# Kernel optimization log

Measured on AMD Instinct MI355X. Metric: run time of the kernel, lower is better.

The kernel has to match this reference:

```python
import jax, jax.numpy as jnp
import numpy as np
from jax import lax

B, C, H, W = 4, 256, 64, 64
R = 4  # reduction
BN_EPS = 1e-5


def setup_inputs() -> dict:
    key = jax.random.key(0)
    ks = jax.random.split(key, 18)
    n = jax.random.normal
    return {
        "x_self": n(ks[0], (B, C, H, W), jnp.float32),
        "x_other": n(ks[1], (B, C, H, W), jnp.float32),
        "q_w": n(ks[2], (C, C), jnp.float32) * 0.05,      # self_q 1x1 conv
        "q_b": n(ks[3], (C,), jnp.float32) * 0.05,
        "kv_w": n(ks[4], (2 * C, C), jnp.float32) * 0.05,  # other_kv 1x1 conv
        "kv_b": n(ks[5], (2 * C,), jnp.float32) * 0.05,
        "g1_w": n(ks[6], (C // R, C), jnp.float32) * 0.05,  # gate conv1
        "g1_b": n(ks[7], (C // R,), jnp.float32) * 0.05,
        "g2_w": n(ks[8], (1, C // R), jnp.float32) * 0.05,  # gate conv2
        "g2_b": n(ks[9], (1,), jnp.float32) * 0.05,
        "dw_w": n(ks[10], (C, 1, 3, 3), jnp.float32) * 0.1,  # depthwise 3x3
        "dw_b": n(ks[11], (C,), jnp.float32) * 0.05,
        "bn_g": jnp.ones((C,), jnp.float32),
        "bn_b": jnp.zeros((C,), jnp.float32),
        "bn_m": n(ks[12], (C,), jnp.float32) * 0.05,
        "bn_v": jax.random.uniform(ks[13], (C,), jnp.float32, 0.5, 1.5),
        "out_w": n(ks[14], (C, C), jnp.float32) * 0.05,
        "out_b": n(ks[15], (C,), jnp.float32) * 0.05,
    }


def _conv1x1(x, w, b):
    return jnp.einsum('bchw,oc->bohw', x, w) + b[None, :, None, None]


def reference(x_self, x_other, q_w, q_b, kv_w, kv_b, g1_w, g1_b, g2_w, g2_b,
              dw_w, dw_b, bn_g, bn_b, bn_m, bn_v, out_w, out_b):
    # local branch: depthwise 3x3 conv -> BatchNorm (eval stats) -> SiLU
    y = lax.conv_general_dilated(
        x_self, dw_w, (1, 1), 'SAME',
        feature_group_count=C,
        dimension_numbers=('NCHW', 'OIHW', 'NCHW')) + dw_b[None, :, None, None]
    scale = (bn_g / jnp.sqrt(bn_v + BN_EPS))[None, :, None, None]
    y = (y - bn_m[None, :, None, None]) * scale + bn_b[None, :, None, None]
    local_feat = y * jax.nn.sigmoid(y)  # SiLU

    # cross attention over HW tokens
    q = _conv1x1(x_self, q_w, q_b).reshape(B, C, H * W)
    kv = _conv1x1(x_other, kv_w, kv_b)
    k = kv[:, :C].reshape(B, C, H * W)
    v = kv[:, C:].reshape(B, C, H * W)
    attn = jnp.einsum('bcn,bcm->bnm', q, k) / jnp.sqrt(jnp.float32(C))  # [B,HW,HW]
    attn = jax.nn.softmax(attn, axis=-1)
    attn_out = jnp.einsum('bnm,bcm->bcn', attn, v).reshape(B, C, H, W)

    # channel-squeeze gate on x_self -> scalar per sample
    p = jnp.mean(x_self, axis=(2, 3))                 # [B,C] global avg pool
    g = jax.nn.relu(p @ g1_w.T + g1_b)                # [B,C//R]
    g = jax.nn.sigmoid(g @ g2_w.T + g2_b)             # [B,1]
    gate = g[:, :, None, None]

    fused = local_feat + gate * attn_out
    return _conv1x1(fused, out_w, out_b)
```

## Files before the change

### kernel.cpp

```cpp
#include <hip/hip_runtime.h>
#include <stdint.h>

#define BB 4
#define CC 256
#define HH 64
#define WWD 64
#define NN 4096
#define LOG2E 1.4426950408889634f

typedef __attribute__((ext_vector_type(8))) short short8;
typedef __attribute__((ext_vector_type(4))) float f32x4;
typedef __attribute__((ext_vector_type(16))) float f32x16;
typedef __attribute__((ext_vector_type(4))) unsigned short us4;
typedef unsigned long long ull;

__device__ __forceinline__ unsigned short f2bf(float f) {
  unsigned int u = __float_as_uint(f);
  u += 0x7fffu + ((u >> 16) & 1u);
  return (unsigned short)(u >> 16);
}
__device__ __forceinline__ float bf2f(unsigned short h) {
  return __uint_as_float(((unsigned int)h) << 16);
}
__device__ __forceinline__ short8 ld8(const unsigned short* p) {
  return *reinterpret_cast<const short8*>(p);
}
__device__ __forceinline__ unsigned char f2fp8(float v) {
  return (unsigned char)__builtin_amdgcn_cvt_pk_fp8_f32(v, v, 0, false);
}
__device__ __forceinline__ int rowmap(int reg, int h) {
  return (reg & 3) + 8 * (reg >> 2) + 4 * h;
}

__global__ __launch_bounds__(256, 2) void k_pre(
    const float* __restrict__ xs, const float* __restrict__ xo,
    const float* __restrict__ dww, const float* __restrict__ dwb,
    const float* __restrict__ bng, const float* __restrict__ bnb,
    const float* __restrict__ bnm, const float* __restrict__ bnv,
    const float* __restrict__ qw, const float* __restrict__ kvw,
    const float* __restrict__ ow, unsigned short* __restrict__ XtS,
    unsigned short* __restrict__ XtO, unsigned short* __restrict__ localT,
    float* __restrict__ psumA, unsigned short* __restrict__ Wb) {
  __shared__ float rb3[3][64][67];
  __shared__ unsigned short sb[64][67];
  int tid = threadIdx.x;
  if (blockIdx.z == 8) {
    int i = (blockIdx.x * 64 + blockIdx.y) * 1024 + tid * 4;
    const float* src;
    if (i < 65536) src = qw + i;
    else if (i < 196608) src = kvw + (i - 65536);
    else src = ow + (i - 196608);
    f32x4 v = *reinterpret_cast<const f32x4*>(src);
    us4 r;
#pragma unroll
    for (int j = 0; j < 4; ++j) r[j] = f2bf(v[j]);
    *reinterpret_cast<us4*>(Wb + i) = r;
    return;
  }
  int c0 = blockIdx.x * 64, h = blockIdx.y;
  int b = blockIdx.z >> 1, which = blockIdx.z & 1;
  const float* src = which ? xo : xs;
  int wq = tid >> 6, w = tid & 63;
  int dlo = which ? 1 : 0, dhi = which ? 1 : 2;
  for (int d = dlo; d <= dhi; ++d) {
    int hh = h + d - 1;
    bool ok = (hh >= 0 && hh < HH);
#pragma unroll
    for (int p = 0; p < 4; ++p) {
      int idx = p * 256 + tid;
      int cl = idx >> 4, ws4 = (idx & 15) * 4;
      f32x4 v = {};
      if (ok)
        v = *reinterpret_cast<const f32x4*>(
            &src[(((size_t)(b * CC + c0 + cl)) * HH + hh) * WWD + ws4]);
#pragma unroll
      for (int j = 0; j < 4; ++j) rb3[d][cl][ws4 + 1 + j] = v[j];
    }
    if (tid < 64) { rb3[d][tid][0] = 0.f; rb3[d][tid][65] = 0.f; }
  }
  __syncthreads();
  unsigned short* dst = which ? XtO : XtS;
  int n0 = h * 64, cb = (tid & 15) * 4;
#pragma unroll
  for (int i = 0; i < 4; ++i) {
    int wl = i * 16 + (tid >> 4);
    us4 r;
#pragma unroll
    for (int j = 0; j < 4; ++j) r[j] = f2bf(rb3[1][cb + j][wl + 1]);
    *reinterpret_cast<us4*>(&dst[((size_t)b * NN + n0 + wl) * CC + c0 + cb]) = r;
  }
  if (which) return;
  if (tid < 64) {
    float s = 0.f;
    for (int ww = 0; ww < 64; ++ww) s += rb3[1][tid][ww + 1];
    psumA[((size_t)(b * 64 + h)) * CC + c0 + tid] = s;
  }
  for (int p = 0; p < 16; ++p) {
    int cl = p * 4 + wq, c = c0 + cl;
    float acc = 0.f;
#pragma unroll
    for (int di = 0; di < 3; ++di)
#pragma unroll
      for (int dj = 0; dj < 3; ++dj)
        acc = fmaf(rb3[di][cl][w + dj], dww[c * 9 + di * 3 + dj], acc);
    float y = acc + dwb[c];
    float sc = bng[c] * rsqrtf(bnv[c] + 1e-5f);
    float v = (y - bnm[c]) * sc + bnb[c];
    sb[cl][w] = f2bf(v / (1.f + __expf(-v)));
  }
  __syncthreads();
#pragma unroll
  for (int i = 0; i < 4; ++i) {
    int wl = i * 16 + (tid >> 4);
    us4 r;
#pragma unroll
    for (int j = 0; j < 4; ++j) r[j] = sb[cb + j][wl];
    *reinterpret_cast<us4*>(&localT[((size_t)b * NN + h * WWD + wl) * CC + c0 + cb]) = r;
  }
}

__global__ __launch_bounds__(256, 4) void k_qkv(
    const unsigned short* __restrict__ XtS, const unsigned short* __restrict__ XtO,
    const unsigned short* __restrict__ Wb, const float* __restrict__ qb,
    const float* __restrict__ kvb, const float* __restrict__ psumA,
    const float* __restrict__ g1w, const float* __restrict__ g1b,
    const float* __restrict__ g2w, const float* __restrict__ g2b,
    unsigned char* __restrict__ Qt8, unsigned char* __restrict__ Kt8,
    unsigned char* __restrict__ Vv8, float* __restrict__ gate) {
  __shared__ unsigned short Xs[64][264];
  int tid = threadIdx.x;
  int id = blockIdx.y;
  if (id == 3) {
    if (blockIdx.x != 0 || blockIdx.z != 0) return;
    float* mf = (float*)&Xs[0][0];
    float* hpf = mf + 1024;
    int c = tid;
    for (int b4 = 0; b4 < 4; ++b4) {
      float s = 0.f;
      for (int hh = 0; hh < 64; ++hh) s += psumA[((size_t)(b4 * 64 + hh)) * CC + c];
      mf[b4 * 256 + c] = s * (1.f / 4096.f);
    }
    __syncthreads();
    for (int b4 = 0; b4 < 4; ++b4) {
      int j = tid >> 2, cq = tid & 3;
      float s = 0.f;
      for (int cc = cq * 64; cc < cq * 64 + 64; ++cc)
        s = fmaf(mf[b4 * 256 + cc], g1w[j * CC + cc], s);
      hpf[j * 5 + cq] = s;
      __syncthreads();
      if (tid < 64) {
        float hh = fmaxf(hpf[tid * 5] + hpf[tid * 5 + 1] + hpf[tid * 5 + 2] +
                             hpf[tid * 5 + 3] + g1b[tid], 0.f);
        float t = hh * g2w[tid];
        for (int off = 32; off; off >>= 1) t += __shfl_down(t, off, 64);
        if (tid == 0) gate[b4] = 1.f / (1.f + expf(-(t + g2b[0])));
      }
      __syncthreads();
    }
    return;
  }
  int n0 = blockIdx.x * 64, b = blockIdx.z;
  const unsigned short* Xt = (id == 0) ? XtS : XtO;
  const unsigned short* W = Wb + id * 65536;
  int wave = tid >> 6, lane = tid & 63, l31 = lane & 31, h = lane >> 5;
#pragma unroll
  for (int p = 0; p < 8; ++p) {
    int r = p * 8 + (tid >> 5), c = (tid & 31) * 8;
    *reinterpret_cast<uint4*>(&Xs[r][c]) =
        *reinterpret_cast<const uint4*>(Xt + ((size_t)b * NN + n0 + r) * CC + c);
  }
  __syncthreads();
  int o0 = wave * 64;
  f32x16 acc[4] = {};
  if (id < 2) {
#pragma unroll
    for (int t = 0; t < 16; ++t) {
      short8 a0 = ld8(&Xs[l31][t * 16 + h * 8]);
      short8 a1 = ld8(&Xs[32 + l31][t * 16 + h * 8]);
      short8 b0 = ld8(W + (size_t)(o0 + l31) * CC + t * 16 + h * 8);
      short8 b1 = ld8(W + (size_t)(o0 + 32 + l31) * CC + t * 16 + h * 8);
      acc[0] = __builtin_amdgcn_mfma_f32_32x32x16_bf16(a0, b0, acc[0], 0, 0, 0);
      acc[1] = __builtin_amdgcn_mfma_f32_32x32x16_bf16(a0, b1, acc[1], 0, 0, 0);
      acc[2] = __builtin_amdgcn_mfma_f32_32x32x16_bf16(a1, b0, acc[2], 0, 0, 0);
      acc[3] = __builtin_amdgcn_mfma_f32_32x32x16_bf16(a1, b1, acc[3], 0, 0, 0);
    }
    const float* bias = id ? kvb : qb;
    __syncthreads();
    unsigned char (*T8)[264] = reinterpret_cast<unsigned char(*)[264]>(&Xs[0][0]);
#pragma unroll
    for (int nt = 0; nt < 2; ++nt)
#pragma unroll
      for (int ot = 0; ot < 2; ++ot) {
        int o = o0 + ot * 32 + l31;
        float bv = bias[o];
#pragma unroll
        for (int reg = 0; reg < 16; ++reg) {
          int nl = nt * 32 + rowmap(reg, h);
          T8[nl][o] = f2fp8((acc[nt * 2 + ot][reg] + bv) * 0.25f);
        }
      }
    __syncthreads();
    if (id == 0) {
#pragma unroll
      for (int p = 0; p < 4; ++p) {
        int idx = p * 256 + tid, row = idx >> 4, cc = (idx & 15) * 16;
        ull a0 = *reinterpret_cast<const ull*>(&T8[row][cc]);
        ull a1 = *reinterpret_cast<const ull*>(&T8[row][cc + 8]);
        uint4 u;
        u.x = (unsigned)a0; u.y = (unsigned)(a0 >> 32);
        u.z = (unsigned)a1; u.w = (unsigned)(a1 >> 32);
        *reinterpret_cast<uint4*>(Qt8 + ((size_t)b * NN + n0 + row) * CC + cc) = u;
      }
    } else {
      size_t tb = ((size_t)b * 32 + (n0 >> 7)) * 32768 + (size_t)(n0 & 64) * 8;
#pragma unroll
      for (int p = 0; p < 8; ++p) {
        int ch = p * 256 + tid;
        int m = ch & 63, s2 = ch >> 6;
        *reinterpret_cast<ull*>(Kt8 + tb + (size_t)s2 * 1024 + m * 8) =
            *reinterpret_cast<const ull*>(&T8[m][s2 * 8]);
      }
    }
  } else {
#pragma unroll
    for (int t = 0; t < 16; ++t) {
      short8 a0 = ld8(W + (size_t)(o0 + l31) * CC + t * 16 + h * 8);
      short8 a1 = ld8(W + (size_t)(o0 + 32 + l31) * CC + t * 16 + h * 8);
      short8 b0 = ld8(&Xs[l31][t * 16 + h * 8]);
      short8 b1 = ld8(&Xs[32 + l31][t * 16 + h * 8]);
      acc[0] = __builtin_amdgcn_mfma_f32_32x32x16_bf16(a0, b0, acc[0], 0, 0, 0);
      acc[1] = __builtin_amdgcn_mfma_f32_32x32x16_bf16(a0, b1, acc[1], 0, 0, 0);
      acc[2] = __builtin_amdgcn_mfma_f32_32x32x16_bf16(a1, b0, acc[2], 0, 0, 0);
      acc[3] = __builtin_amdgcn_mfma_f32_32x32x16_bf16(a1, b1, acc[3], 0, 0, 0);
    }
    __syncthreads();
    unsigned char (*V8)[72] = reinterpret_cast<unsigned char(*)[72]>(&Xs[0][0]);
#pragma unroll
    for (int ot = 0; ot < 2; ++ot)
#pragma unroll
      for (int nt = 0; nt < 2; ++nt)
#pragma unroll
        for (int reg = 0; reg < 16; ++reg) {
          int o = o0 + ot * 32 + rowmap(reg, h);
          int nl = nt * 32 + l31;
          V8[o][nl] = f2fp8(acc[ot * 2 + nt][reg] + kvb[CC + o]);
        }
    __syncthreads();
    size_t tb = ((size_t)b * 32 + (n0 >> 7)) * 32768 + (size_t)((n0 & 64) >> 3) * 2048;
#pragma unroll
    for (int p = 0; p < 8; ++p) {
      int ch = p * 256 + tid;
      int c = ch & 255, svl = ch >> 8;
      *reinterpret_cast<ull*>(Vv8 + tb + (size_t)svl * 2048 + c * 8) =
          *reinterpret_cast<const ull*>(&V8[c][svl * 8]);
    }
  }
}

__global__ __launch_bounds__(256, 3) void k_flash8(
    const unsigned char* __restrict__ Qt8, const unsigned char* __restrict__ Kd,
    const unsigned char* __restrict__ Vd, const unsigned short* __restrict__ localT,
    const float* __restrict__ gate, unsigned short* __restrict__ OpartA,
    unsigned short* __restrict__ OpartB,
    float* __restrict__ Lpart, unsigned short* __restrict__ fusedT) {
  __shared__ unsigned char Ps8[64][136];
  __shared__ float lred[2][64];
  int b = blockIdx.x & 3, n0 = (blockIdx.x >> 2) * 64;
  int sp = blockIdx.y, nsp = gridDim.y;
  int tid = threadIdx.x, wave = tid >> 6, lane = tid & 63, l31 = lane & 31, h = lane >> 5;
  int rw = wave & 1, cw = wave >> 1;
  const unsigned char* qp = Qt8 + ((size_t)b * NN + n0 + rw * 32 + l31) * CC + h * 8;
  long qf[16];
#pragma unroll
  for (int t = 0; t < 16; ++t) qf[t] = *reinterpret_cast<const long*>(qp + t * 16);
  f32x16 O[4] = {};
  float lsum = 0.f;
  int m_lo = (32 * sp) / nsp, m_hi = (32 * (sp + 1)) / nsp;
  const unsigned char* Kb = Kd + (size_t)b * (32u * 32768u);
  const unsigned char* Vb = Vd + (size_t)b * (32u * 32768u);
  for (int mt = m_lo; mt < m_hi; ++mt) {
    const unsigned char* Kq = Kb + (size_t)mt * 32768 + h * 1024 + (cw * 64 + l31) * 8;
    f32x16 Sa = {}, Sb = {};
    __builtin_amdgcn_s_setprio(1);
#pragma unroll
    for (int t = 0; t < 16; ++t) {
      long kfa = *reinterpret_cast<const long*>(Kq + (size_t)t * 2048);
      long kfb = *reinterpret_cast<const long*>(Kq + (size_t)t * 2048 + 256);
      Sa = __builtin_amdgcn_mfma_f32_32x32x16_fp8_fp8(kfa, qf[t], Sa, 0, 0, 0);
      Sb = __builtin_amdgcn_mfma_f32_32x32x16_fp8_fp8(kfb, qf[t], Sb, 0, 0, 0);
    }
    __builtin_amdgcn_s_setprio(0);
#pragma unroll
    for (int r = 0; r < 4; ++r) {
      float p0 = __builtin_exp2f(Sa[4 * r + 0] * LOG2E);
      float p1 = __builtin_exp2f(Sa[4 * r + 1] * LOG2E);
      float p2 = __builtin_exp2f(Sa[4 * r + 2] * LOG2E);
      float p3 = __builtin_exp2f(Sa[4 * r + 3] * LOG2E);
      lsum += (p0 + p1) + (p2 + p3);
      unsigned u = __builtin_amdgcn_cvt_pk_fp8_f32(p0, p1, 0, false);
      u = __builtin_amdgcn_cvt_pk_fp8_f32(p2, p3, u, true);
      *reinterpret_cast<unsigned*>(&Ps8[rw * 32 + l31][cw * 64 + 8 * r + 4 * h]) = u;
      float q0 = __builtin_exp2f(Sb[4 * r + 0] * LOG2E);
      float q1 = __builtin_exp2f(Sb[4 * r + 1] * LOG2E);
      float q2 = __builtin_exp2f(Sb[4 * r + 2] * LOG2E);
      float q3 = __builtin_exp2f(Sb[4 * r + 3] * LOG2E);
      lsum += (q0 + q1) + (q2 + q3);
      unsigned u2 = __builtin_amdgcn_cvt_pk_fp8_f32(q0, q1, 0, false);
      u2 = __builtin_amdgcn_cvt_pk_fp8_f32(q2, q3, u2, true);
      *reinterpret_cast<unsigned*>(&Ps8[rw * 32 + l31][cw * 64 + 32 + 8 * r + 4 * h]) = u2;
    }
    asm volatile("s_waitcnt lgkmcnt(0)" ::: "memory");
    __builtin_amdgcn_s_barrier();
    __builtin_amdgcn_sched_barrier(0);
    const unsigned char* Vq = Vb + (size_t)mt * 32768 + h * 2048 + (cw * 128 + l31) * 8;
    __builtin_amdgcn_s_setprio(1);
#pragma unroll
    for (int t = 0; t < 8; ++t) {
      long pf = *reinterpret_cast<const long*>(&Ps8[rw * 32 + l31][t * 16 + h * 8]);
#pragma unroll
      for (int ct = 0; ct < 4; ++ct) {
        long vf = *reinterpret_cast<const long*>(Vq + (size_t)t * 4096 + ct * 256);
        O[ct] = __builtin_amdgcn_mfma_f32_32x32x16_fp8_fp8(pf, vf, O[ct], 0, 0, 0);
      }
    }
    __builtin_amdgcn_s_setprio(0);
    __builtin_amdgcn_s_barrier();
  }
  lsum += __shfl_xor(lsum, 32, 64);
  __syncthreads();
  if (h == 0) lred[cw][rw * 32 + l31] = lsum;
  __syncthreads();
  if (nsp == 1) {
    float* ltot = reinterpret_cast<float*>(&Ps8[0][0]);
    if (tid < 64) ltot[tid] = lred[0][tid] + lred[1][tid];
    __syncthreads();
    float gv = gate[b];
    float inv[16];
#pragma unroll
    for (int reg = 0; reg < 16; ++reg)
      inv[reg] = gv / ltot[rw * 32 + rowmap(reg, h)];
#pragma unroll
    for (int ct = 0; ct < 4; ++ct)
#pragma unroll
      for (int reg = 0; reg < 16; ++reg) {
        int n = n0 + rw * 32 + rowmap(reg, h);
        int c = cw * 128 + ct * 32 + l31;
        size_t idx = ((size_t)b * NN + n) * CC + c;
        fusedT[idx] = f2bf(bf2f(localT[idx]) + O[ct][reg] * inv[reg]);
      }
  } else {
    if (tid < 64) Lpart[(size_t)(b * nsp + sp) * NN + n0 + tid] = lred[0][tid] + lred[1][tid];
    unsigned short* Op;
    size_t slab;
    if (sp == 0) { Op = OpartA; slab = (size_t)b * NN; }
    else { Op = OpartB; slab = (size_t)(b * (nsp - 1) + (sp - 1)) * NN; }
#pragma unroll
    for (int ct = 0; ct < 4; ++ct)
#pragma unroll
      for (int reg = 0; reg < 16; ++reg) {
        int n = n0 + rw * 32 + rowmap(reg, h);
        int c = cw * 128 + ct * 32 + l31;
        Op[(slab + n) * CC + c] = f2bf(O[ct][reg]);
      }
  }
}

__global__ __launch_bounds__(256, 4) void k_out(
    const unsigned short* __restrict__ W, const float* __restrict__ ob,
    const float* __restrict__ gate, const unsigned short* __restrict__ localT,
    const unsigned short* __restrict__ OpartA, const unsigned short* __restrict__ OpartB,
    const float* __restrict__ Lpart,
    const unsigned short* __restrict__ fusedT, float* __restrict__ out, int nsp) {
  __shared__ unsigned short Xs[64][264];
  int n0 = blockIdx.x * 64, o0 = blockIdx.y * 128, b = blockIdx.z;
  int tid = threadIdx.x, wave = tid >> 6, lane = tid & 63, l31 = lane & 31, h = lane >> 5;
  if (nsp > 1) {
    float gv = gate[b];
#pragma unroll
    for (int p = 0; p < 8; ++p) {
      int r = p * 8 + (tid >> 5), cc = (tid & 31) * 8;
      int n = n0 + r;
      float lsum = 0.f;
      for (int sp = 0; sp < nsp; ++sp) lsum += Lpart[(size_t)(b * nsp + sp) * NN + n];
      float g = gv / lsum;
      float ov[8] = {};
      for (int sp = 0; sp < nsp; ++sp) {
        const unsigned short* Op;
        size_t slab;
        if (sp == 0) { Op = OpartA; slab = (size_t)b * NN; }
        else { Op = OpartB; slab = (size_t)(b * (nsp - 1) + (sp - 1)) * NN; }
        short8 x = ld8(Op + (slab + n) * CC + cc);
#pragma unroll
        for (int j = 0; j < 8; ++j) ov[j] += bf2f(((unsigned short*)&x)[j]);
      }
      const unsigned short* lp = localT + ((size_t)b * NN + n) * CC + cc;
      short8 lv = ld8(lp);
      us4 r0, r1;
#pragma unroll
      for (int j = 0; j < 4; ++j) {
        r0[j] = f2bf(bf2f(((unsigned short*)&lv)[j]) + ov[j] * g);
        r1[j] = f2bf(bf2f(((unsigned short*)&lv)[j + 4]) + ov[j + 4] * g);
      }
      *reinterpret_cast<us4*>(&Xs[r][cc]) = r0;
      *reinterpret_cast<us4*>(&Xs[r][cc + 4]) = r1;
    }
  } else {
#pragma unroll
    for (int p = 0; p < 8; ++p) {
      int r = p * 8 + (tid >> 5), c = (tid & 31) * 8;
      *reinterpret_cast<uint4*>(&Xs[r][c]) =
          *reinterpret_cast<const uint4*>(fusedT + ((size_t)b * NN + n0 + r) * CC + c);
    }
  }
  int obase = o0 + wave * 32;
  short8 af[16];
#pragma unroll
  for (int t = 0; t < 16; ++t) af[t] = ld8(W + (size_t)(obase + l31) * CC + t * 16 + h * 8);
  __syncthreads();
  f32x16 acc[2] = {};
#pragma unroll
  for (int t = 0; t < 16; ++t) {
    short8 b0 = ld8(&Xs[l31][t * 16 + h * 8]);
    short8 b1 = ld8(&Xs[32 + l31][t * 16 + h * 8]);
    acc[0] = __builtin_amdgcn_mfma_f32_32x32x16_bf16(af[t], b0, acc[0], 0, 0, 0);
    acc[1] = __builtin_amdgcn_mfma_f32_32x32x16_bf16(af[t], b1, acc[1], 0, 0, 0);
  }
#pragma unroll
  for (int nt = 0; nt < 2; ++nt)
#pragma unroll
    for (int reg = 0; reg < 16; ++reg) {
      int o = obase + rowmap(reg, h);
      int n = n0 + nt * 32 + l31;
      out[((size_t)b * CC + o) * NN + n] = acc[nt][reg] + ob[o];
    }
}

extern "C" void kernel_launch(void* const* d_in, const int* in_sizes, int n_in,
                              void* d_out, int out_size, void* d_ws, size_t ws_size,
                              hipStream_t stream) {
  const float* xs  = (const float*)d_in[0];
  const float* xo  = (const float*)d_in[1];
  const float* qw  = (const float*)d_in[2];
  const float* qb  = (const float*)d_in[3];
  const float* kvw = (const float*)d_in[4];
  const float* kvb = (const float*)d_in[5];
  const float* g1w = (const float*)d_in[6];
  const float* g1b = (const float*)d_in[7];
  const float* g2w = (const float*)d_in[8];
  const float* g2b = (const float*)d_in[9];
  const float* dww = (const float*)d_in[10];
  const float* dwb = (const float*)d_in[11];
  const float* bng = (const float*)d_in[12];
  const float* bnb = (const float*)d_in[13];
  const float* bnm = (const float*)d_in[14];
  const float* bnv = (const float*)d_in[15];
  const float* ow  = (const float*)d_in[16];
  const float* ob  = (const float*)d_in[17];
  float* out = (float*)d_out;
  char* ws = (char*)d_ws;

  const size_t SZ  = (size_t)BB * NN * CC * 2;
  const size_t SZ8 = (size_t)BB * NN * CC;
  unsigned short* XtS    = (unsigned short*)(ws);
  unsigned short* XtO    = (unsigned short*)(ws + SZ);
  unsigned short* localT = (unsigned short*)(ws + 2 * SZ);
  unsigned char*  Qt8    = (unsigned char*)(ws + 3 * SZ);
  unsigned char*  Kt8    = (unsigned char*)(ws + 3 * SZ + SZ8);
  unsigned char*  Vv8    = (unsigned char*)(ws + 3 * SZ + 2 * SZ8);
  unsigned short* Wb     = (unsigned short*)(ws + 3 * SZ + 3 * SZ8);
  float* psumA = (float*)(ws + 3 * SZ + 3 * SZ8 + 524288);
  float* gate  = (float*)(ws + 3 * SZ + 3 * SZ8 + 524288 + 262144);
  size_t tail  = 3 * SZ + 3 * SZ8 + 524288 + 262144 + 4096;
  float* Lpart = (float*)(ws + tail);
  unsigned short* OpartA = XtO;
  unsigned short* OpartB = (unsigned short*)(ws + tail + 262144);
  unsigned short* fusedT = XtS;

  size_t base = tail + 262144;
  int S = 1;
  if (ws_size >= base + 2ull * SZ) S = 3;
  else if (ws_size >= base + 1ull * SZ) S = 2;

  k_pre<<<dim3(4, 64, 9), 256, 0, stream>>>(xs, xo, dww, dwb, bng, bnb, bnm, bnv,
                                            qw, kvw, ow, XtS, XtO, localT, psumA, Wb);
  k_qkv<<<dim3(64, 4, 4), 256, 0, stream>>>(XtS, XtO, Wb, qb, kvb, psumA,
                                            g1w, g1b, g2w, g2b, Qt8, Kt8, Vv8, gate);
  k_flash8<<<dim3(256, S), 256, 0, stream>>>(Qt8, Kt8, Vv8, localT, gate, OpartA,
                                             OpartB, Lpart, fusedT);
  k_out<<<dim3(64, 2, 4), 256, 0, stream>>>(Wb + 196608, ob, gate, localT,
                                            OpartA, OpartB, Lpart, fusedT, out, S);
}
```

Before: 250.9 us.

## Feed P directly from registers to PV MFMA and double-buffer the exchange tile

The V tile layout written by the KV projection kernel is permuted so that the S-accumulator register layout of each wave can be used directly as the A operand of the PV MFMA. Each wave multiplies its own P half straight from registers and reads only the other wave's half from double-buffered shared memory. This removes one barrier per tile and half of the LDS round trip for P. In exchange it depends on a subtle permutation of the key index staying consistent between the producer and consumer kernels, and it raises shared memory use.

```diff
diff --git a/kernel.cpp b/kernel.cpp
--- a/kernel.cpp
+++ b/kernel.cpp
@@ -246,13 +246,16 @@
           V8[o][nl] = f2fp8(acc[ot * 2 + nt][reg] + kvb[CC + o]);
         }
     __syncthreads();
-    size_t tb = ((size_t)b * 32 + (n0 >> 7)) * 32768 + (size_t)((n0 & 64) >> 3) * 2048;
+    size_t tb = ((size_t)b * 32 + (n0 >> 7)) * 32768 + (size_t)(n0 & 64) * 256;
 #pragma unroll
     for (int p = 0; p < 8; ++p) {
       int ch = p * 256 + tid;
-      int c = ch & 255, svl = ch >> 8;
-      *reinterpret_cast<ull*>(Vv8 + tb + (size_t)svl * 2048 + c * 8) =
-          *reinterpret_cast<const ull*>(&V8[c][svl * 8]);
+      int c = ch & 255, slot = ch >> 8;
+      int tl = slot >> 1, h2 = slot & 1;
+      unsigned lo = *reinterpret_cast<const unsigned*>(&V8[c][tl * 16 + h2 * 4]);
+      unsigned hi = *reinterpret_cast<const unsigned*>(&V8[c][tl * 16 + 8 + h2 * 4]);
+      ull chunk = (ull)lo | ((ull)hi << 32);
+      *reinterpret_cast<ull*>(Vv8 + tb + (size_t)slot * 2048 + c * 8) = chunk;
     }
   }
 }
@@ -263,7 +266,7 @@
     const float* __restrict__ gate, unsigned short* __restrict__ OpartA,
     unsigned short* __restrict__ OpartB,
     float* __restrict__ Lpart, unsigned short* __restrict__ fusedT) {
-  __shared__ unsigned char Ps8[64][136];
+  __shared__ unsigned char PsD[2][2][2][64][32];
   __shared__ float lred[2][64];
   int b = blockIdx.x & 3, n0 = (blockIdx.x >> 2) * 64;
   int sp = blockIdx.y, nsp = gridDim.y;
@@ -278,6 +281,7 @@
   int m_lo = (32 * sp) / nsp, m_hi = (32 * (sp + 1)) / nsp;
   const unsigned char* Kb = Kd + (size_t)b * (32u * 32768u);
   const unsigned char* Vb = Vd + (size_t)b * (32u * 32768u);
+  int buf = 0;
   for (int mt = m_lo; mt < m_hi; ++mt) {
     const unsigned char* Kq = Kb + (size_t)mt * 32768 + h * 1024 + (cw * 64 + l31) * 8;
     f32x16 Sa = {}, Sb = {};
@@ -290,48 +294,99 @@
       Sb = __builtin_amdgcn_mfma_f32_32x32x16_fp8_fp8(kfb, qf[t], Sb, 0, 0, 0);
     }
     __builtin_amdgcn_s_setprio(0);
-#pragma unroll
-    for (int r = 0; r < 4; ++r) {
-      float p0 = __builtin_exp2f(Sa[4 * r + 0] * LOG2E);
-      float p1 = __builtin_exp2f(Sa[4 * r + 1] * LOG2E);
-      float p2 = __builtin_exp2f(Sa[4 * r + 2] * LOG2E);
-      float p3 = __builtin_exp2f(Sa[4 * r + 3] * LOG2E);
-      lsum += (p0 + p1) + (p2 + p3);
-      unsigned u = __builtin_amdgcn_cvt_pk_fp8_f32(p0, p1, 0, false);
-      u = __builtin_amdgcn_cvt_pk_fp8_f32(p2, p3, u, true);
-      *reinterpret_cast<unsigned*>(&Ps8[rw * 32 + l31][cw * 64 + 8 * r + 4 * h]) = u;
-      float q0 = __builtin_exp2f(Sb[4 * r + 0] * LOG2E);
-      float q1 = __builtin_exp2f(Sb[4 * r + 1] * LOG2E);
-      float q2 = __builtin_exp2f(Sb[4 * r + 2] * LOG2E);
-      float q3 = __builtin_exp2f(Sb[4 * r + 3] * LOG2E);
-      lsum += (q0 + q1) + (q2 + q3);
-      unsigned u2 = __builtin_amdgcn_cvt_pk_fp8_f32(q0, q1, 0, false);
-      u2 = __builtin_amdgcn_cvt_pk_fp8_f32(q2, q3, u2, true);
-      *reinterpret_cast<unsigned*>(&Ps8[rw * 32 + l31][cw * 64 + 32 + 8 * r + 4 * h]) = u2;
-    }
+    unsigned d0, d1, d2, d3, d4, d5, d6, d7;
+    {
+      float e0 = __builtin_exp2f(Sa[0] * LOG2E), e1 = __builtin_exp2f(Sa[1] * LOG2E);
+      float e2 = __builtin_exp2f(Sa[2] * LOG2E), e3 = __builtin_exp2f(Sa[3] * LOG2E);
+      lsum += (e0 + e1) + (e2 + e3);
+      d0 = __builtin_amdgcn_cvt_pk_fp8_f32(e2, e3,
+           __builtin_amdgcn_cvt_pk_fp8_f32(e0, e1, 0, false), true);
+      e0 = __builtin_exp2f(Sa[4] * LOG2E); e1 = __builtin_exp2f(Sa[5] * LOG2E);
+      e2 = __builtin_exp2f(Sa[6] * LOG2E); e3 = __builtin_exp2f(Sa[7] * LOG2E);
+      lsum += (e0 + e1) + (e2 + e3);
+      d1 = __builtin_amdgcn_cvt_pk_fp8_f32(e2, e3,
+           __builtin_amdgcn_cvt_pk_fp8_f32(e0, e1, 0, false), true);
+      e0 = __builtin_exp2f(Sa[8] * LOG2E); e1 = __builtin_exp2f(Sa[9] * LOG2E);
+      e2 = __builtin_exp2f(Sa[10] * LOG2E); e3 = __builtin_exp2f(Sa[11] * LOG2E);
+      lsum += (e0 + e1) + (e2 + e3);
+      d2 = __builtin_amdgcn_cvt_pk_fp8_f32(e2, e3,
+           __builtin_amdgcn_cvt_pk_fp8_f32(e0, e1, 0, false), true);
+      e0 = __builtin_exp2f(Sa[12] * LOG2E); e1 = __builtin_exp2f(Sa[13] * LOG2E);
+      e2 = __builtin_exp2f(Sa[14] * LOG2E); e3 = __builtin_exp2f(Sa[15] * LOG2E);
+      lsum += (e0 + e1) + (e2 + e3);
+      d3 = __builtin_amdgcn_cvt_pk_fp8_f32(e2, e3,
+           __builtin_amdgcn_cvt_pk_fp8_f32(e0, e1, 0, false), true);
+      e0 = __builtin_exp2f(Sb[0] * LOG2E); e1 = __builtin_exp2f(Sb[1] * LOG2E);
+      e2 = __builtin_exp2f(Sb[2] * LOG2E); e3 = __builtin_exp2f(Sb[3] * LOG2E);
+      lsum += (e0 + e1) + (e2 + e3);
+      d4 = __builtin_amdgcn_cvt_pk_fp8_f32(e2, e3,
+           __builtin_amdgcn_cvt_pk_fp8_f32(e0, e1, 0, false), true);
+      e0 = __builtin_exp2f(Sb[4] * LOG2E); e1 = __builtin_exp2f(Sb[5] * LOG2E);
+      e2 = __builtin_exp2f(Sb[6] * LOG2E); e3 = __builtin_exp2f(Sb[7] * LOG2E);
+      lsum += (e0 + e1) + (e2 + e3);
+      d5 = __builtin_amdgcn_cvt_pk_fp8_f32(e2, e3,
+           __builtin_amdgcn_cvt_pk_fp8_f32(e0, e1, 0, false), true);
+      e0 = __builtin_exp2f(Sb[8] * LOG2E); e1 = __builtin_exp2f(Sb[9] * LOG2E);
+      e2 = __builtin_exp2f(Sb[10] * LOG2E); e3 = __builtin_exp2f(Sb[11] * LOG2E);
+      lsum += (e0 + e1) + (e2 + e3);
+      d6 = __builtin_amdgcn_cvt_pk_fp8_f32(e2, e3,
+           __builtin_amdgcn_cvt_pk_fp8_f32(e0, e1, 0, false), true);
+      e0 = __builtin_exp2f(Sb[12] * LOG2E); e1 = __builtin_exp2f(Sb[13] * LOG2E);
+      e2 = __builtin_exp2f(Sb[14] * LOG2E); e3 = __builtin_exp2f(Sb[15] * LOG2E);
+      lsum += (e0 + e1) + (e2 + e3);
+      d7 = __builtin_amdgcn_cvt_pk_fp8_f32(e2, e3,
+           __builtin_amdgcn_cvt_pk_fp8_f32(e0, e1, 0, false), true);
+    }
+    uint4 w0; w0.x = d0; w0.y = d1; w0.z = d2; w0.w = d3;
+    uint4 w1; w1.x = d4; w1.y = d5; w1.z = d6; w1.w = d7;
+    *reinterpret_cast<uint4*>(&PsD[buf][cw][rw][lane][0]) = w0;
+    *reinterpret_cast<uint4*>(&PsD[buf][cw][rw][lane][16]) = w1;
+    const unsigned char* Vq = Vb + (size_t)mt * 32768 + h * 2048 + (cw * 128 + l31) * 8;
+    long pf0 = (long)(((ull)d1 << 32) | d0);
+    long pf1 = (long)(((ull)d3 << 32) | d2);
+    long pf2 = (long)(((ull)d5 << 32) | d4);
+    long pf3 = (long)(((ull)d7 << 32) | d6);
+    __builtin_amdgcn_s_setprio(1);
+#pragma unroll
+    for (int ct = 0; ct < 4; ++ct) {
+      const unsigned char* Vc = Vq + (size_t)(cw * 4) * 4096 + ct * 256;
+      O[ct] = __builtin_amdgcn_mfma_f32_32x32x16_fp8_fp8(
+          pf0, *reinterpret_cast<const long*>(Vc), O[ct], 0, 0, 0);
+      O[ct] = __builtin_amdgcn_mfma_f32_32x32x16_fp8_fp8(
+          pf1, *reinterpret_cast<const long*>(Vc + 4096), O[ct], 0, 0, 0);
+      O[ct] = __builtin_amdgcn_mfma_f32_32x32x16_fp8_fp8(
+          pf2, *reinterpret_cast<const long*>(Vc + 8192), O[ct], 0, 0, 0);
+      O[ct] = __builtin_amdgcn_mfma_f32_32x32x16_fp8_fp8(
+          pf3, *reinterpret_cast<const long*>(Vc + 12288), O[ct], 0, 0, 0);
+    }
+    __builtin_amdgcn_s_setprio(0);
     asm volatile("s_waitcnt lgkmcnt(0)" ::: "memory");
     __builtin_amdgcn_s_barrier();
     __builtin_amdgcn_sched_barrier(0);
-    const unsigned char* Vq = Vb + (size_t)mt * 32768 + h * 2048 + (cw * 128 + l31) * 8;
+    const ull* pp = reinterpret_cast<const ull*>(&PsD[buf][cw ^ 1][rw][lane][0]);
+    ull q0 = pp[0], q1 = pp[1], q2 = pp[2], q3 = pp[3];
     __builtin_amdgcn_s_setprio(1);
 #pragma unroll
-    for (int t = 0; t < 8; ++t) {
-      long pf = *reinterpret_cast<const long*>(&Ps8[rw * 32 + l31][t * 16 + h * 8]);
-#pragma unroll
-      for (int ct = 0; ct < 4; ++ct) {
-        long vf = *reinterpret_cast<const long*>(Vq + (size_t)t * 4096 + ct * 256);
-        O[ct] = __builtin_amdgcn_mfma_f32_32x32x16_fp8_fp8(pf, vf, O[ct], 0, 0, 0);
-      }
+    for (int ct = 0; ct < 4; ++ct) {
+      const unsigned char* Vc = Vq + (size_t)((cw ^ 1) * 4) * 4096 + ct * 256;
+      O[ct] = __builtin_amdgcn_mfma_f32_32x32x16_fp8_fp8(
+          (long)q0, *reinterpret_cast<const long*>(Vc), O[ct], 0, 0, 0);
+      O[ct] = __builtin_amdgcn_mfma_f32_32x32x16_fp8_fp8(
+          (long)q1, *reinterpret_cast<const long*>(Vc + 4096), O[ct], 0, 0, 0);
+      O[ct] = __builtin_amdgcn_mfma_f32_32x32x16_fp8_fp8(
+          (long)q2, *reinterpret_cast<const long*>(Vc + 8192), O[ct], 0, 0, 0);
+      O[ct] = __builtin_amdgcn_mfma_f32_32x32x16_fp8_fp8(
+          (long)q3, *reinterpret_cast<const long*>(Vc + 12288), O[ct], 0, 0, 0);
     }
     __builtin_amdgcn_s_setprio(0);
-    __builtin_amdgcn_s_barrier();
+    buf ^= 1;
   }
   lsum += __shfl_xor(lsum, 32, 64);
   __syncthreads();
   if (h == 0) lred[cw][rw * 32 + l31] = lsum;
   __syncthreads();
   if (nsp == 1) {
-    float* ltot = reinterpret_cast<float*>(&Ps8[0][0]);
+    float* ltot = reinterpret_cast<float*>(&PsD[0][0][0][0][0]);
     if (tid < 64) ltot[tid] = lred[0][tid] + lred[1][tid];
     __syncthreads();
     float gv = gate[b];
```

Measured after the change: 276.7 us. 1.1x slower.
